# Kernel tuning notes

Measured on AMD Instinct MI355X. Metric: run time of the kernel, lower is better.

The kernel has to match this reference:

```python
import jax, jax.numpy as jnp
import numpy as np

DIM = 768
HEADS = 12
D_HEAD = DIM // HEADS
SCALE = DIM ** (-0.5)  # note: full dimension, matching original code


def setup_inputs() -> dict:
    key = jax.random.key(0)
    k1, k2, k3, k4 = jax.random.split(key, 4)
    x = jax.random.normal(k1, (8, 1024, DIM), dtype=jnp.float32)
    w_in = jax.random.normal(k2, (DIM, 3 * DIM), dtype=jnp.float32) * (DIM ** -0.5)
    w_out = jax.random.normal(k3, (DIM, DIM), dtype=jnp.float32) * (DIM ** -0.5)
    b_out = jax.random.normal(k4, (DIM,), dtype=jnp.float32) * 0.01
    return {"x": x, "w_in": w_in, "w_out": w_out, "b_out": b_out}


def reference(x, w_in, w_out, b_out):
    b, n, _ = x.shape
    qkv = x @ w_in  # [b, n, 3*dim]
    # 'b n (qkv h d) -> qkv b h n d'
    qkv = qkv.reshape(b, n, 3, HEADS, D_HEAD).transpose(2, 0, 3, 1, 4)
    q, k, v = qkv[0], qkv[1], qkv[2]
    scores = jnp.einsum('bhid,bhjd->bhij', q, k) * SCALE
    attn = jax.nn.softmax(scores, axis=-1)
    out = jnp.einsum('bhij,bhjd->bhid', attn, v)  # [b, h, n, d]
    out = out.transpose(0, 2, 1, 3).reshape(b, n, DIM)  # 'b h n d -> b n (h d)'
    return out @ w_out + b_out
```

## Files before the change

kernel.cpp:

```cpp
#include <hip/hip_runtime.h>


using short8 = __attribute__((ext_vector_type(8))) short;
using s16x4  = __attribute__((ext_vector_type(4))) short;
using f32x4  = __attribute__((ext_vector_type(4))) float;

#define MFMA_B16(a, b, c) __builtin_amdgcn_mfma_f32_16x16x32_bf16((a), (b), (c), 0, 0, 0)

typedef const __attribute__((address_space(1))) void* gvoid_p;
typedef __attribute__((address_space(3))) void* lvoid_p;

constexpr int   kDim   = 768;
constexpr int   kHeads = 12;
constexpr int   kSeq   = 1024;
constexpr float kScale = 0.03608439182435161f;
constexpr float kQSc   = kScale * 1.4426950408889634f;

__device__ __forceinline__ short f2bf(float f) {
  unsigned u = __float_as_uint(f);
  u += 0x7FFFu + ((u >> 16) & 1u);
  return (short)(u >> 16);
}
__device__ __forceinline__ unsigned cvt_pk_bf16(float lo, float hi) {
  unsigned r;
  asm("v_cvt_pk_bf16_f32 %0, %1, %2" : "=v"(r) : "v"(lo), "v"(hi));
  return r;
}
union U8 { unsigned u[4]; short8 s; };

__global__ __launch_bounds__(256) void cvt_f32_bf16(const float* __restrict__ in,
                                                    short* __restrict__ out) {
  const int i = blockIdx.x * 256 + threadIdx.x;
  float4 a = ((const float4*)in)[i * 2];
  float4 b = ((const float4*)in)[i * 2 + 1];
  short8 s;
  s[0] = f2bf(a.x); s[1] = f2bf(a.y); s[2] = f2bf(a.z); s[3] = f2bf(a.w);
  s[4] = f2bf(b.x); s[5] = f2bf(b.y); s[6] = f2bf(b.z); s[7] = f2bf(b.w);
  ((short8*)out)[i] = s;
}

__global__ __launch_bounds__(256) void transpose_cvt(const float* __restrict__ in,
                                                     short* __restrict__ out,
                                                     int R, int C) {
  __shared__ float tile[32][33];
  const int c0 = blockIdx.x * 32, r0 = blockIdx.y * 32;
  const int tx = threadIdx.x & 31, ty = threadIdx.x >> 5;
#pragma unroll
  for (int i = 0; i < 32; i += 8)
    tile[ty + i][tx] = in[(size_t)(r0 + ty + i) * C + c0 + tx];
  __syncthreads();
#pragma unroll
  for (int i = 0; i < 32; i += 8)
    out[(size_t)(c0 + ty + i) * R + r0 + tx] = f2bf(tile[tx][ty + i]);
}

template <int EPI>
__global__ __launch_bounds__(256) void gemm_tile(const short* __restrict__ A,
                                                 const short* __restrict__ BT,
                                                 int Kd,
                                                 short* __restrict__ Qb,
                                                 short* __restrict__ Kb,
                                                 short* __restrict__ VTb,
                                                 const float* __restrict__ bias,
                                                 float* __restrict__ outF) {
  __shared__ short As[2][128 * 32];
  __shared__ short Bs[2][128 * 32];

  const int tid  = threadIdx.x;
  const int lane = tid & 63, w = tid >> 6;
  const int L = lane & 15, g = lane >> 4;
  const int wr = w >> 1, wc = w & 1;
  const int m0 = blockIdx.x * 128, n0 = blockIdx.y * 128;

  const int r4 = lane >> 2;
  const int c8 = (lane & 3) * 8;

  auto stage = [&](int buf, int k0) {
#pragma unroll
    for (int c = 0; c < 2; ++c) {
      const short* ag = A  + (size_t)(m0 + w * 32 + c * 16 + r4) * Kd + k0 + c8;
      const short* bg = BT + (size_t)(n0 + w * 32 + c * 16 + r4) * Kd + k0 + c8;
      __builtin_amdgcn_global_load_lds((gvoid_p)ag, (lvoid_p)&As[buf][(w * 2 + c) * 512], 16, 0, 0);
      __builtin_amdgcn_global_load_lds((gvoid_p)bg, (lvoid_p)&Bs[buf][(w * 2 + c) * 512], 16, 0, 0);
    }
  };

  f32x4 acc[4][4] = {};

  stage(0, 0);
  __syncthreads();

  const int NT = Kd / 32;
  for (int t = 0; t < NT; ++t) {
    const int cur = t & 1;
    if (t + 1 < NT) stage(cur ^ 1, (t + 1) * 32);

    short8 af[4], bfr[4];
#pragma unroll
    for (int mi = 0; mi < 4; ++mi)
      af[mi] = *(const short8*)&As[cur][(wr * 64 + mi * 16 + L) * 32 + g * 8];
#pragma unroll
    for (int ni = 0; ni < 4; ++ni)
      bfr[ni] = *(const short8*)&Bs[cur][(wc * 64 + ni * 16 + L) * 32 + g * 8];
#pragma unroll
    for (int mi = 0; mi < 4; ++mi)
#pragma unroll
      for (int ni = 0; ni < 4; ++ni)
        acc[mi][ni] = MFMA_B16(af[mi], bfr[ni], acc[mi][ni]);

    __syncthreads();
  }

  if (EPI == 0) {
    const int t3 = n0 / kDim;
#pragma unroll
    for (int mi = 0; mi < 4; ++mi) {
#pragma unroll
      for (int ni = 0; ni < 4; ++ni) {
        const int gcol = n0 + wc * 64 + ni * 16 + L;
        const int hd = gcol % kDim;
        const int h = hd >> 6, d = hd & 63;
        if (t3 == 2) {
          const int grow = m0 + wr * 64 + mi * 16 + 4 * g;
          const int b = grow >> 10, seq = grow & 1023;
          const int bh = b * kHeads + h;
          uint2 d2;
          d2.x = cvt_pk_bf16(acc[mi][ni][0], acc[mi][ni][1]);
          d2.y = cvt_pk_bf16(acc[mi][ni][2], acc[mi][ni][3]);
          *(uint2*)&VTb[((size_t)bh * 64 + d) * kSeq + seq] = d2;
        } else {
#pragma unroll
          for (int r = 0; r < 4; ++r) {
            const int grow = m0 + wr * 64 + mi * 16 + 4 * g + r;
            const int b = grow >> 10, seq = grow & 1023;
            const int bh = b * kHeads + h;
            if (t3 == 0) Qb[((size_t)bh * kSeq + seq) * 64 + d] = f2bf(acc[mi][ni][r] * kQSc);
            else         Kb[((size_t)bh * kSeq + seq) * 64 + d] = f2bf(acc[mi][ni][r]);
          }
        }
      }
    }
  } else {
#pragma unroll
    for (int ni = 0; ni < 4; ++ni) {
      const int gcol = n0 + wc * 64 + ni * 16 + L;
      const float bv = bias[gcol];
#pragma unroll
      for (int mi = 0; mi < 4; ++mi) {
#pragma unroll
        for (int r = 0; r < 4; ++r) {
          const int grow = m0 + wr * 64 + mi * 16 + 4 * g + r;
          outF[(size_t)grow * kDim + gcol] = acc[mi][ni][r] + bv;
        }
      }
    }
  }
}

__global__ __launch_bounds__(256) void attn_kernel(const short* __restrict__ Qb,
                                                   const short* __restrict__ Kb,
                                                   const short* __restrict__ VTb,
                                                   short* __restrict__ AO) {
  __shared__ short Ks[2][64 * 72];
  __shared__ short VTs[2][64 * 72];

  const int tid  = threadIdx.x;
  const int lane = tid & 63, w = tid >> 6;
  const int L = lane & 15, g = lane >> 4;
  const int id = blockIdx.x;
  const int bh = id % 96, qc = id / 96;
  const int q0 = qc * 128 + w * 32;

  const short* Qbase = Qb  + (size_t)bh * kSeq * 64;
  const short* Kbase = Kb  + (size_t)bh * kSeq * 64;
  const short* Vbase = VTb + (size_t)bh * 64 * kSeq;

  short8 qf[2][2];
#pragma unroll
  for (int qh = 0; qh < 2; ++qh) {
    const short* qp = Qbase + (size_t)(q0 + qh * 16 + L) * 64 + g * 8;
    qf[qh][0] = *(const short8*)qp;
    qf[qh][1] = *(const short8*)(qp + 32);
  }

  f32x4 o[2][4] = {};
  float m_[2] = {-1e30f, -1e30f};
  float l_[2] = {0.f, 0.f};

  const int srow = tid >> 2, sc0 = (tid & 3) * 16;

  {
    const short* ksrc = Kbase + (size_t)srow * 64 + sc0;
    const short* vsrc = Vbase + (size_t)srow * kSeq + sc0;
    uint4 k0 = ((const uint4*)ksrc)[0], k1 = ((const uint4*)ksrc)[1];
    uint4 v0 = ((const uint4*)vsrc)[0], v1 = ((const uint4*)vsrc)[1];
    *(uint4*)&Ks[0][srow * 72 + sc0]      = k0;
    *(uint4*)&Ks[0][srow * 72 + sc0 + 8]  = k1;
    *(uint4*)&VTs[0][srow * 72 + sc0]     = v0;
    *(uint4*)&VTs[0][srow * 72 + sc0 + 8] = v1;
  }
  __syncthreads();

  for (int t = 0; t < kSeq / 64; ++t) {
    const int cur = t & 1;
    const bool pf = (t + 1 < kSeq / 64);

    uint4 kr0, kr1, vr0, vr1;
    if (pf) {
      const int kv1 = (t + 1) * 64;
      const short* ksrc = Kbase + (size_t)(kv1 + srow) * 64 + sc0;
      const short* vsrc = Vbase + (size_t)srow * kSeq + kv1 + sc0;
      kr0 = ((const uint4*)ksrc)[0]; kr1 = ((const uint4*)ksrc)[1];
      vr0 = ((const uint4*)vsrc)[0]; vr1 = ((const uint4*)vsrc)[1];
    }

    short8 kf[4][2];
#pragma unroll
    for (int nf = 0; nf < 4; ++nf) {
      const short* kp = &Ks[cur][(nf * 16 + L) * 72 + g * 8];
      kf[nf][0] = *(const short8*)kp;
      kf[nf][1] = *(const short8*)(kp + 32);
    }
    short8 vb[4][2];
#pragma unroll
    for (int nf = 0; nf < 4; ++nf) {
      const short* vrow = &VTs[cur][(nf * 16 + L) * 72];
      s16x4 a0 = *(const s16x4*)&vrow[4 * g];
      s16x4 a1 = *(const s16x4*)&vrow[16 + 4 * g];
      s16x4 a2 = *(const s16x4*)&vrow[32 + 4 * g];
      s16x4 a3 = *(const s16x4*)&vrow[48 + 4 * g];
      vb[nf][0] = __builtin_shufflevector(a0, a1, 0, 1, 2, 3, 4, 5, 6, 7);
      vb[nf][1] = __builtin_shufflevector(a2, a3, 0, 1, 2, 3, 4, 5, 6, 7);
    }

    short8 pa[2][2];
#pragma unroll
    for (int qh = 0; qh < 2; ++qh) {
      f32x4 s[4];
      __builtin_amdgcn_s_setprio(1);
#pragma unroll
      for (int nf = 0; nf < 4; ++nf) {
        f32x4 z = {};
        z = MFMA_B16(kf[nf][0], qf[qh][0], z);
        s[nf] = MFMA_B16(kf[nf][1], qf[qh][1], z);
      }
      __builtin_amdgcn_s_setprio(0);

      float x0 = fmaxf(fmaxf(s[0][0], s[0][1]), fmaxf(s[0][2], s[0][3]));
      float x1 = fmaxf(fmaxf(s[1][0], s[1][1]), fmaxf(s[1][2], s[1][3]));
      float x2 = fmaxf(fmaxf(s[2][0], s[2][1]), fmaxf(s[2][2], s[2][3]));
      float x3 = fmaxf(fmaxf(s[3][0], s[3][1]), fmaxf(s[3][2], s[3][3]));
      const float mt4 = fmaxf(fmaxf(x0, x1), fmaxf(x2, x3));

      if (__any(mt4 > m_[qh] + 8.0f)) {
        float mt = fmaxf(mt4, __shfl_xor(mt4, 16, 64));
        mt = fmaxf(mt, __shfl_xor(mt, 32, 64));
        const float mnew = fmaxf(m_[qh], mt);
        const float al = __builtin_amdgcn_exp2f(m_[qh] - mnew);
        m_[qh] = mnew;
        l_[qh] *= al;
        float alr[4];
#pragma unroll
        for (int r = 0; r < 4; ++r) alr[r] = __shfl(al, 4 * g + r, 64);
#pragma unroll
        for (int nf = 0; nf < 4; ++nf)
#pragma unroll
          for (int r = 0; r < 4; ++r) o[qh][nf][r] *= alr[r];
      }

      float rsum = 0.f;
#pragma unroll
      for (int nf = 0; nf < 4; ++nf) {
#pragma unroll
        for (int r = 0; r < 4; ++r) {
          const float p = __builtin_amdgcn_exp2f(s[nf][r] - m_[qh]);
          s[nf][r] = p;
          rsum += p;
        }
      }
      l_[qh] += rsum;

      U8 t0, t1;
      t0.u[0] = cvt_pk_bf16(s[0][0], s[0][1]);
      t0.u[1] = cvt_pk_bf16(s[0][2], s[0][3]);
      t0.u[2] = cvt_pk_bf16(s[1][0], s[1][1]);
      t0.u[3] = cvt_pk_bf16(s[1][2], s[1][3]);
      t1.u[0] = cvt_pk_bf16(s[2][0], s[2][1]);
      t1.u[1] = cvt_pk_bf16(s[2][2], s[2][3]);
      t1.u[2] = cvt_pk_bf16(s[3][0], s[3][1]);
      t1.u[3] = cvt_pk_bf16(s[3][2], s[3][3]);
      pa[qh][0] = t0.s;
      pa[qh][1] = t1.s;
    }

    __builtin_amdgcn_s_setprio(1);
#pragma unroll
    for (int nf = 0; nf < 4; ++nf) {
#pragma unroll
      for (int qh = 0; qh < 2; ++qh) {
        o[qh][nf] = MFMA_B16(pa[qh][0], vb[nf][0], o[qh][nf]);
        o[qh][nf] = MFMA_B16(pa[qh][1], vb[nf][1], o[qh][nf]);
      }
    }
    __builtin_amdgcn_s_setprio(0);

    if (pf) {
      *(uint4*)&Ks[cur ^ 1][srow * 72 + sc0]      = kr0;
      *(uint4*)&Ks[cur ^ 1][srow * 72 + sc0 + 8]  = kr1;
      *(uint4*)&VTs[cur ^ 1][srow * 72 + sc0]     = vr0;
      *(uint4*)&VTs[cur ^ 1][srow * 72 + sc0 + 8] = vr1;
    }
    __syncthreads();
  }

  const int b = bh / kHeads, h = bh % kHeads;
#pragma unroll
  for (int qh = 0; qh < 2; ++qh) {
    float ls = l_[qh] + __shfl_xor(l_[qh], 16, 64);
    ls += __shfl_xor(ls, 32, 64);
    float lq[4];
#pragma unroll
    for (int r = 0; r < 4; ++r) lq[r] = __shfl(ls, 4 * g + r, 64);
    short* aop = AO + ((size_t)(b * kSeq) + q0 + qh * 16) * kDim + h * 64;
#pragma unroll
    for (int r = 0; r < 4; ++r) {
      const float inv = 1.0f / lq[r];
#pragma unroll
      for (int nf = 0; nf < 4; ++nf)
        aop[(size_t)(4 * g + r) * kDim + nf * 16 + L] = f2bf(o[qh][nf][r] * inv);
    }
  }
}

extern "C" void kernel_launch(void* const* d_in, const int* in_sizes, int n_in,
                              void* d_out, int out_size, void* d_ws, size_t ws_size,
                              hipStream_t stream) {
  const float* x     = (const float*)d_in[0];
  const float* w_in  = (const float*)d_in[1];
  const float* w_out = (const float*)d_in[2];
  const float* b_out = (const float*)d_in[3];
  float* out = (float*)d_out;

  short* WinT  = (short*)d_ws;
  short* WoutT = WinT  + (size_t)2304 * 768;
  short* Qb    = WoutT + (size_t)768 * 768;
  short* Kb    = Qb    + (size_t)96 * 1024 * 64;
  short* VTb   = Kb    + (size_t)96 * 1024 * 64;
  short* AO    = VTb   + (size_t)96 * 1024 * 64;
  short* xbf   = AO;

  cvt_f32_bf16<<<dim3(8192 * 768 / (256 * 8)), 256, 0, stream>>>(x, xbf);
  transpose_cvt<<<dim3(2304 / 32, 768 / 32), 256, 0, stream>>>(w_in, WinT, 768, 2304);
  transpose_cvt<<<dim3(768 / 32, 768 / 32), 256, 0, stream>>>(w_out, WoutT, 768, 768);

  gemm_tile<0><<<dim3(8192 / 128, 2304 / 128), 256, 0, stream>>>(
      xbf, WinT, 768, Qb, Kb, VTb, nullptr, nullptr);

  attn_kernel<<<dim3(768), 256, 0, stream>>>(Qb, Kb, VTb, AO);

  gemm_tile<1><<<dim3(8192 / 128, 768 / 128), 256, 0, stream>>>(
      AO, WoutT, 768, nullptr, nullptr, nullptr, b_out, out);
}
```

Baseline: 127.4 us.

## Double GEMM K-tile to 64 and read attention V directly from global

The GEMM kernel now stages 64-wide K slices instead of 32, halving the loop trips and barriers and issuing twice as many MFMAs per tile. LDS use per block doubles to 64 KB, which can lower occupancy. The attention kernel no longer stages V^T through shared memory and loads its 8-byte fragments straight from global memory each iteration. That removes the LDS traffic and some register pressure for V, but puts uncoalesced, unprefetched global loads on the critical path, relying on caches.

After: 201.2 us. +57.9%, slower.

```diff
diff --git a/kernel.cpp b/kernel.cpp
--- a/kernel.cpp
+++ b/kernel.cpp
@@ -63,8 +63,8 @@
                                                  short* __restrict__ VTb,
                                                  const float* __restrict__ bias,
                                                  float* __restrict__ outF) {
-  __shared__ short As[2][128 * 32];
-  __shared__ short Bs[2][128 * 32];
+  __shared__ short As[2][128 * 64];
+  __shared__ short Bs[2][128 * 64];
 
   const int tid  = threadIdx.x;
   const int lane = tid & 63, w = tid >> 6;
@@ -72,16 +72,17 @@
   const int wr = w >> 1, wc = w & 1;
   const int m0 = blockIdx.x * 128, n0 = blockIdx.y * 128;
 
-  const int r4 = lane >> 2;
-  const int c8 = (lane & 3) * 8;
+  const int r8 = lane >> 3;
+  const int c8 = (lane & 7) * 8;
 
   auto stage = [&](int buf, int k0) {
 #pragma unroll
-    for (int c = 0; c < 2; ++c) {
-      const short* ag = A  + (size_t)(m0 + w * 32 + c * 16 + r4) * Kd + k0 + c8;
-      const short* bg = BT + (size_t)(n0 + w * 32 + c * 16 + r4) * Kd + k0 + c8;
-      __builtin_amdgcn_global_load_lds((gvoid_p)ag, (lvoid_p)&As[buf][(w * 2 + c) * 512], 16, 0, 0);
-      __builtin_amdgcn_global_load_lds((gvoid_p)bg, (lvoid_p)&Bs[buf][(w * 2 + c) * 512], 16, 0, 0);
+    for (int c = 0; c < 4; ++c) {
+      const int row = w * 32 + c * 8;
+      const short* ag = A  + (size_t)(m0 + row + r8) * Kd + k0 + c8;
+      const short* bg = BT + (size_t)(n0 + row + r8) * Kd + k0 + c8;
+      __builtin_amdgcn_global_load_lds((gvoid_p)ag, (lvoid_p)&As[buf][row * 64], 16, 0, 0);
+      __builtin_amdgcn_global_load_lds((gvoid_p)bg, (lvoid_p)&Bs[buf][row * 64], 16, 0, 0);
     }
   };
 
@@ -90,23 +91,28 @@
   stage(0, 0);
   __syncthreads();
 
-  const int NT = Kd / 32;
+  const int NT = Kd / 64;
   for (int t = 0; t < NT; ++t) {
     const int cur = t & 1;
-    if (t + 1 < NT) stage(cur ^ 1, (t + 1) * 32);
-
-    short8 af[4], bfr[4];
-#pragma unroll
-    for (int mi = 0; mi < 4; ++mi)
-      af[mi] = *(const short8*)&As[cur][(wr * 64 + mi * 16 + L) * 32 + g * 8];
-#pragma unroll
-    for (int ni = 0; ni < 4; ++ni)
-      bfr[ni] = *(const short8*)&Bs[cur][(wc * 64 + ni * 16 + L) * 32 + g * 8];
-#pragma unroll
-    for (int mi = 0; mi < 4; ++mi)
+    if (t + 1 < NT) stage(cur ^ 1, (t + 1) * 64);
+
+    short8 af[2][4], bfr[2][4];
+#pragma unroll
+    for (int kk = 0; kk < 2; ++kk) {
+#pragma unroll
+      for (int mi = 0; mi < 4; ++mi)
+        af[kk][mi] = *(const short8*)&As[cur][(wr * 64 + mi * 16 + L) * 64 + kk * 32 + g * 8];
 #pragma unroll
       for (int ni = 0; ni < 4; ++ni)
-        acc[mi][ni] = MFMA_B16(af[mi], bfr[ni], acc[mi][ni]);
+        bfr[kk][ni] = *(const short8*)&Bs[cur][(wc * 64 + ni * 16 + L) * 64 + kk * 32 + g * 8];
+    }
+#pragma unroll
+    for (int kk = 0; kk < 2; ++kk)
+#pragma unroll
+      for (int mi = 0; mi < 4; ++mi)
+#pragma unroll
+        for (int ni = 0; ni < 4; ++ni)
+          acc[mi][ni] = MFMA_B16(af[kk][mi], bfr[kk][ni], acc[mi][ni]);
 
     __syncthreads();
   }
@@ -162,7 +168,6 @@
                                                    const short* __restrict__ VTb,
                                                    short* __restrict__ AO) {
   __shared__ short Ks[2][64 * 72];
-  __shared__ short VTs[2][64 * 72];
 
   const int tid  = threadIdx.x;
   const int lane = tid & 63, w = tid >> 6;
@@ -191,27 +196,22 @@
 
   {
     const short* ksrc = Kbase + (size_t)srow * 64 + sc0;
-    const short* vsrc = Vbase + (size_t)srow * kSeq + sc0;
     uint4 k0 = ((const uint4*)ksrc)[0], k1 = ((const uint4*)ksrc)[1];
-    uint4 v0 = ((const uint4*)vsrc)[0], v1 = ((const uint4*)vsrc)[1];
-    *(uint4*)&Ks[0][srow * 72 + sc0]      = k0;
-    *(uint4*)&Ks[0][srow * 72 + sc0 + 8]  = k1;
-    *(uint4*)&VTs[0][srow * 72 + sc0]     = v0;
-    *(uint4*)&VTs[0][srow * 72 + sc0 + 8] = v1;
+    *(uint4*)&Ks[0][srow * 72 + sc0]     = k0;
+    *(uint4*)&Ks[0][srow * 72 + sc0 + 8] = k1;
   }
   __syncthreads();
 
   for (int t = 0; t < kSeq / 64; ++t) {
     const int cur = t & 1;
+    const int kv0 = t * 64;
     const bool pf = (t + 1 < kSeq / 64);
 
-    uint4 kr0, kr1, vr0, vr1;
+    uint4 kr0, kr1;
     if (pf) {
-      const int kv1 = (t + 1) * 64;
-      const short* ksrc = Kbase + (size_t)(kv1 + srow) * 64 + sc0;
-      const short* vsrc = Vbase + (size_t)srow * kSeq + kv1 + sc0;
-      kr0 = ((const uint4*)ksrc)[0]; kr1 = ((const uint4*)ksrc)[1];
-      vr0 = ((const uint4*)vsrc)[0]; vr1 = ((const uint4*)vsrc)[1];
+      const short* ksrc = Kbase + (size_t)(kv0 + 64 + srow) * 64 + sc0;
+      kr0 = ((const uint4*)ksrc)[0];
+      kr1 = ((const uint4*)ksrc)[1];
     }
 
     short8 kf[4][2];
@@ -224,7 +224,7 @@
     short8 vb[4][2];
 #pragma unroll
     for (int nf = 0; nf < 4; ++nf) {
-      const short* vrow = &VTs[cur][(nf * 16 + L) * 72];
+      const short* vrow = Vbase + (size_t)(nf * 16 + L) * kSeq + kv0;
       s16x4 a0 = *(const s16x4*)&vrow[4 * g];
       s16x4 a1 = *(const s16x4*)&vrow[16 + 4 * g];
       s16x4 a2 = *(const s16x4*)&vrow[32 + 4 * g];
@@ -305,10 +305,8 @@
     __builtin_amdgcn_s_setprio(0);
 
     if (pf) {
-      *(uint4*)&Ks[cur ^ 1][srow * 72 + sc0]      = kr0;
-      *(uint4*)&Ks[cur ^ 1][srow * 72 + sc0 + 8]  = kr1;
-      *(uint4*)&VTs[cur ^ 1][srow * 72 + sc0]     = vr0;
-      *(uint4*)&VTs[cur ^ 1][srow * 72 + sc0 + 8] = vr1;
+      *(uint4*)&Ks[cur ^ 1][srow * 72 + sc0]     = kr0;
+      *(uint4*)&Ks[cur ^ 1][srow * 72 + sc0 + 8] = kr1;
     }
     __syncthreads();
   }
```
